# Kernel tuning notes

Hardware: AMD Instinct MI355X
Metric: run time of the kernel (lower is better)

The kernel has to match this reference:

```python
import jax, jax.numpy as jnp
import numpy as np

B, S, E = 2, 2048, 1024
H, D = 16, 64


def setup_inputs() -> dict:
    key = jax.random.key(0)
    ks = jax.random.split(key, 9)
    s_in = 1.0 / np.sqrt(E)
    s_out = 1.0 / np.sqrt(H * D)
    return {
        "x": jax.random.normal(ks[0], (B, S, E), dtype=jnp.float32),
        "W_q": jax.random.uniform(ks[1], (H, E, D), jnp.float32, -s_in, s_in),
        "b_q": jax.random.uniform(ks[2], (H, D), jnp.float32, -s_in, s_in),
        "W_k": jax.random.uniform(ks[3], (H, E, D), jnp.float32, -s_in, s_in),
        "b_k": jax.random.uniform(ks[4], (H, D), jnp.float32, -s_in, s_in),
        "W_v": jax.random.uniform(ks[5], (H, E, D), jnp.float32, -s_in, s_in),
        "b_v": jax.random.uniform(ks[6], (H, D), jnp.float32, -s_in, s_in),
        "W_o": jax.random.uniform(ks[7], (H * D, E), jnp.float32, -s_out, s_out),
        "b_o": jax.random.uniform(ks[8], (E,), jnp.float32, -s_out, s_out),
    }


def reference(x, W_q, b_q, W_k, b_k, W_v, b_v, W_o, b_o):
    # batched per-head projections: [B,S,E] x [H,E,D] -> [B,H,S,D]
    q = jnp.einsum("bse,hed->bhsd", x, W_q) + b_q[None, :, None, :]
    k = jnp.einsum("bse,hed->bhsd", x, W_k) + b_k[None, :, None, :]
    v = jnp.einsum("bse,hed->bhsd", x, W_v) + b_v[None, :, None, :]
    scale = 1.0 / jnp.sqrt(jnp.asarray(D, dtype=x.dtype))
    score = jnp.einsum("bhsd,bhtd->bhst", q, k) * scale  # [B,H,S,S]
    causal = jnp.tril(jnp.ones((S, S), dtype=bool))
    score = jnp.where(causal[None, None], score, -jnp.inf)
    w = jax.nn.softmax(score, axis=-1)
    o = jnp.einsum("bhst,bhtd->bhsd", w, v)  # [B,H,S,D]
    # concat heads along last dim (head-major order matches torch.cat)
    o = o.transpose(0, 2, 1, 3).reshape(B, S, H * D)
    # dropout is identity in eval mode
    return o @ W_o + b_o
```

## Files before the change

kernel.cpp:

```cpp
#include <hip/hip_runtime.h>


typedef __attribute__((ext_vector_type(8)))  __bf16 bf16x8;
typedef __attribute__((ext_vector_type(4)))  __bf16 bf16x4;
typedef __attribute__((ext_vector_type(2)))  __bf16 bf16x2;
typedef __attribute__((ext_vector_type(4)))  float  f32x4;
typedef __attribute__((ext_vector_type(16))) float  f32x16;
typedef __attribute__((ext_vector_type(2)))  unsigned int u32x2;
typedef __attribute__((ext_vector_type(4)))  unsigned int u32x4;

#define LOG2E 1.4426950408889634f
#define SM_SC (0.125f * LOG2E)
#define MBIAS (32.0f * SM_SC)

static __device__ __forceinline__ void gl2lds16(const void* g, void* l) {
    __builtin_amdgcn_global_load_lds(
        (__attribute__((address_space(1))) void*)(void*)g,
        (__attribute__((address_space(3))) void*)l, 16, 0, 0);
}

static __device__ __forceinline__ unsigned pku(float a, float b) {
    bf16x2 t = { (__bf16)a, (__bf16)b };
    return __builtin_bit_cast(unsigned, t);
}

__global__ void __launch_bounds__(256)
prep_all_kern(const float* __restrict__ x, const float* __restrict__ Wq,
              const float* __restrict__ Wk, const float* __restrict__ Wv,
              const float* __restrict__ bq, const float* __restrict__ bk,
              const float* __restrict__ bv, const float* __restrict__ Wo,
              __bf16* __restrict__ xb, __bf16* __restrict__ wt,
              float* __restrict__ bias, __bf16* __restrict__ wto) {
    __shared__ float T[64][65];
    const int t = threadIdx.x;
    const int bx = blockIdx.x;
    if (bx < 4096) {
        int i = (bx * 256 + t) * 4;
        f32x4 v = *(const f32x4*)(x + i);
        bf16x4 o = { (__bf16)v[0], (__bf16)v[1], (__bf16)v[2], (__bf16)v[3] };
        *(bf16x4*)(xb + i) = o;
    } else if (bx < 4864) {
        const int blk = bx - 4096;
        const int kt = blk & 15, ph = blk >> 4;
        const int h = ph & 15, p = ph >> 4;
        const float* W  = (p == 0) ? Wq : (p == 1) ? Wk : Wv;
        const float* bb = (p == 0) ? bq : (p == 1) ? bk : bv;
        #pragma unroll
        for (int i = 0; i < 4; ++i) {
            int flat = i * 1024 + t * 4;
            int kr = flat >> 6, d4 = flat & 63;
            f32x4 v = *(const f32x4*)(W + (h << 16) + ((kt * 64 + kr) << 6) + d4);
            T[kr][d4] = v[0]; T[kr][d4 + 1] = v[1]; T[kr][d4 + 2] = v[2]; T[kr][d4 + 3] = v[3];
        }
        __syncthreads();
        const int d = t >> 2, kq = (t & 3) << 4;
        bf16x8 o0, o1;
        #pragma unroll
        for (int j = 0; j < 8; ++j) o0[j] = (__bf16)T[kq + j][d];
        #pragma unroll
        for (int j = 0; j < 8; ++j) o1[j] = (__bf16)T[kq + 8 + j][d];
        __bf16* dst = wt + (((size_t)(p * 1024 + h * 64 + d)) << 10) + kt * 64 + kq;
        *(bf16x8*)dst = o0;
        *(bf16x8*)(dst + 8) = o1;
        if (kt == 0 && t < 64) bias[p * 1024 + h * 64 + t] = bb[h * 64 + t];
    } else {
        const int blk = bx - 4864;
        const int nt = blk & 15, ktile = blk >> 4;
        #pragma unroll
        for (int i = 0; i < 4; ++i) {
            int flat = i * 1024 + t * 4;
            int kr = flat >> 6, n4 = flat & 63;
            f32x4 v = *(const f32x4*)(Wo + ((size_t)(ktile * 64 + kr) << 10) + nt * 64 + n4);
            T[kr][n4] = v[0]; T[kr][n4 + 1] = v[1]; T[kr][n4 + 2] = v[2]; T[kr][n4 + 3] = v[3];
        }
        __syncthreads();
        const int n = t >> 2, kq = (t & 3) << 4;
        bf16x8 o0, o1;
        #pragma unroll
        for (int j = 0; j < 8; ++j) o0[j] = (__bf16)T[kq + j][n];
        #pragma unroll
        for (int j = 0; j < 8; ++j) o1[j] = (__bf16)T[kq + 8 + j][n];
        __bf16* dst = wto + (((size_t)(nt * 64 + n)) << 10) + ktile * 64 + kq;
        *(bf16x8*)dst = o0;
        *(bf16x8*)(dst + 8) = o1;
    }
}

template <int EPI>
__global__ void __launch_bounds__(256, 3)
gemm_bt(const __bf16* __restrict__ A, const __bf16* __restrict__ Bt,
        const float* __restrict__ bias,
        __bf16* __restrict__ outq, __bf16* __restrict__ outk, __bf16* __restrict__ outv,
        float* __restrict__ outf)
{
    __shared__ __align__(16) __bf16 As[128 * 64];
    __shared__ __align__(16) __bf16 Bs[128 * 64];
    const int tid = threadIdx.x;
    const int wid = tid >> 6, lane = tid & 63;
    const int r = lane & 15, g = lane >> 4;
    const int m0 = blockIdx.y << 7, n0 = blockIdx.x << 7;
    const int wr = wid >> 1, wc = wid & 1;
    f32x4 acc[4][4] = {};
    for (int k0 = 0; k0 < 1024; k0 += 64) {
        #pragma unroll
        for (int c = 0; c < 4; ++c) {
            int cq = (c * 4 + wid) * 64 + lane;
            int row = cq >> 3, ci = cq & 7;
            gl2lds16(A  + (((size_t)(m0 + row)) << 10) + k0 + ci * 8, As + (c * 4 + wid) * 512);
            gl2lds16(Bt + (((size_t)(n0 + row)) << 10) + k0 + ci * 8, Bs + (c * 4 + wid) * 512);
        }
        __syncthreads();
        bf16x8 af[2][4], bfr[2][4];
        #pragma unroll
        for (int kh = 0; kh < 2; ++kh)
            #pragma unroll
            for (int i = 0; i < 4; ++i) {
                af[kh][i]  = *(const bf16x8*)&As[(wr * 64 + i * 16 + r) * 64 + kh * 32 + g * 8];
                bfr[kh][i] = *(const bf16x8*)&Bs[(wc * 64 + i * 16 + r) * 64 + kh * 32 + g * 8];
            }
        #pragma unroll
        for (int kh = 0; kh < 2; ++kh)
            #pragma unroll
            for (int mi = 0; mi < 4; ++mi)
                #pragma unroll
                for (int ni = 0; ni < 4; ++ni)
                    acc[mi][ni] = __builtin_amdgcn_mfma_f32_16x16x32_bf16(
                        af[kh][mi], bfr[kh][ni], acc[mi][ni], 0, 0, 0);
        __syncthreads();
    }
    if (EPI == 0) {
        #pragma unroll
        for (int ni = 0; ni < 4; ++ni) {
            int n = n0 + wc * 64 + ni * 16 + r;
            float bv = bias[n];
            int p = n >> 10, rem = n & 1023, h = rem >> 6, d = rem & 63;
            #pragma unroll
            for (int mi = 0; mi < 4; ++mi) {
                int mb = m0 + wr * 64 + mi * 16 + g * 4;
                int b = mb >> 11, s = mb & 2047;
                f32x4 v = acc[mi][ni];
                if (p < 2) {
                    __bf16* dst = (p == 0) ? outq : outk;
                    size_t base = (((size_t)(b * 16 + h)) * 2048 + s) * 64 + d;
                    #pragma unroll
                    for (int j = 0; j < 4; ++j)
                        dst[base + (size_t)j * 64] = (__bf16)(v[j] + bv);
                } else {
                    bf16x4 pk = { (__bf16)(v[0] + bv), (__bf16)(v[1] + bv),
                                  (__bf16)(v[2] + bv), (__bf16)(v[3] + bv) };
                    *(bf16x4*)&outv[(((size_t)(b * 16 + h)) * 64 + d) * 2048 + s] = pk;
                }
            }
        }
    } else {
        #pragma unroll
        for (int ni = 0; ni < 4; ++ni) {
            int n = n0 + wc * 64 + ni * 16 + r;
            float bv = bias[n];
            #pragma unroll
            for (int mi = 0; mi < 4; ++mi) {
                int mb = m0 + wr * 64 + mi * 16 + g * 4;
                f32x4 v = acc[mi][ni];
                #pragma unroll
                for (int j = 0; j < 4; ++j)
                    outf[((size_t)(mb + j) << 10) + n] = v[j] + bv;
            }
        }
    }
}

__global__ void __launch_bounds__(256, 3)
attn_kern(const __bf16* __restrict__ q, const __bf16* __restrict__ k,
          const __bf16* __restrict__ vT, __bf16* __restrict__ pO0,
          __bf16* __restrict__ pO1, __bf16* __restrict__ pO2,
          __bf16* __restrict__ pO3, float* __restrict__ ml)
{
    __shared__ __align__(16) __bf16 Ks [2][64][72];
    __shared__ __align__(16) __bf16 VsT[2][64][72];
    const int tid = threadIdx.x, lane = tid & 63, w = tid >> 6;
    const int r31 = lane & 31, hi = lane >> 5;
    const int bid = blockIdx.x;
    const int rnk = bid >> 5, bh = bid & 31;
    const int j = 15 - (rnk >> 2), kvq = rnk & 3;
    const int b = bh >> 4, h = bh & 15;
    const __bf16* qh  = q  + ((size_t)bh << 17);
    const __bf16* khp = k  + ((size_t)bh << 17);
    const __bf16* vhp = vT + ((size_t)bh << 17);
    __bf16* pO = (kvq == 0) ? pO0 : (kvq == 1) ? pO1 : (kvq == 2) ? pO2 : pO3;
    const int srow = tid >> 3, sci = tid & 7;

    const int qb0 = j << 7;
    const int wrow0 = qb0 + w * 32;
    const int mg = wrow0 + r31;
    const int c2 = 2 * (j + 1);
    const int base = c2 >> 2, rem = c2 & 3;
    const int len = base + (kvq < rem ? 1 : 0);
    const int tbeg = kvq * base + min(kvq, rem);
    const int tend = tbeg + len;

    f32x16 oacc[2] = {};
    f32x16 lacc = {};

    if (len > 0) {
        bf16x8 qf[4];
        #pragma unroll
        for (int kk = 0; kk < 4; ++kk)
            qf[kk] = *(const bf16x8*)&qh[(size_t)mg * 64 + kk * 16 + hi * 8];
        bf16x8 onesf;
        #pragma unroll
        for (int jj = 0; jj < 8; ++jj) onesf[jj] = (__bf16)1.0f;

        #pragma unroll
        for (int it = 0; it < 2; ++it) {
            int row = srow + it * 32;
            *(bf16x8*)&Ks [0][row][sci * 8] = *(const bf16x8*)&khp[(size_t)(tbeg * 64 + row) * 64 + sci * 8];
            *(bf16x8*)&VsT[0][row][sci * 8] = *(const bf16x8*)&vhp[(size_t)row * 2048 + tbeg * 64 + sci * 8];
        }
        __syncthreads();

        for (int t = tbeg; t < tend; ++t) {
            const int cur = (t - tbeg) & 1, nxt = cur ^ 1;
            const int n0 = t << 6;
            const bool pre = (t + 1 < tend);
            bf16x8 nk[2], nv[2];
            if (pre) {
                int n1 = n0 + 64;
                #pragma unroll
                for (int it = 0; it < 2; ++it) {
                    int row = srow + it * 32;
                    nk[it] = *(const bf16x8*)&khp[(size_t)(n1 + row) * 64 + sci * 8];
                    nv[it] = *(const bf16x8*)&vhp[(size_t)row * 2048 + n1 + sci * 8];
                }
            }
            if (n0 <= wrow0 + 31) {
                f32x16 sacc[2] = {};
                #pragma unroll
                for (int kk = 0; kk < 4; ++kk) {
                    bf16x8 kf0 = *(const bf16x8*)&Ks[cur][r31]     [kk * 16 + hi * 8];
                    bf16x8 kf1 = *(const bf16x8*)&Ks[cur][32 + r31][kk * 16 + hi * 8];
                    sacc[0] = __builtin_amdgcn_mfma_f32_32x32x16_bf16(kf0, qf[kk], sacc[0], 0, 0, 0);
                    sacc[1] = __builtin_amdgcn_mfma_f32_32x32x16_bf16(kf1, qf[kk], sacc[1], 0, 0, 0);
                }
                if (n0 + 63 > wrow0) {
                    #pragma unroll
                    for (int nf = 0; nf < 2; ++nf)
                        #pragma unroll
                        for (int i = 0; i < 16; ++i) {
                            int n = n0 + nf * 32 + (i & 3) + 8 * (i >> 2) + 4 * hi;
                            if (n > mg) sacc[nf][i] = -3.0e38f;
                        }
                }
                #pragma unroll
                for (int nf = 0; nf < 2; ++nf)
                    #pragma unroll
                    for (int i = 0; i < 16; ++i)
                        sacc[nf][i] = exp2f(fmaf(sacc[nf][i], SM_SC, -MBIAS));
                #pragma unroll
                for (int nf = 0; nf < 2; ++nf) {
                    unsigned pk[8];
                    #pragma unroll
                    for (int jj = 0; jj < 8; ++jj)
                        pk[jj] = pku(sacc[nf][2 * jj], sacc[nf][2 * jj + 1]);
#if __has_builtin(__builtin_amdgcn_permlane32_swap)
                    u32x2 s02 = __builtin_amdgcn_permlane32_swap(pk[0], pk[2], false, false);
                    u32x2 s13 = __builtin_amdgcn_permlane32_swap(pk[1], pk[3], false, false);
                    u32x2 s46 = __builtin_amdgcn_permlane32_swap(pk[4], pk[6], false, false);
                    u32x2 s57 = __builtin_amdgcn_permlane32_swap(pk[5], pk[7], false, false);
                    u32x4 fw0 = { s02[0], s13[0], s02[1], s13[1] };
                    u32x4 fw1 = { s46[0], s57[0], s46[1], s57[1] };
#else
                    unsigned rxa = __shfl_xor(hi ? pk[0] : pk[2], 32);
                    unsigned rxb = __shfl_xor(hi ? pk[1] : pk[3], 32);
                    unsigned rxc = __shfl_xor(hi ? pk[4] : pk[6], 32);
                    unsigned rxd = __shfl_xor(hi ? pk[5] : pk[7], 32);
                    u32x4 fw0 = { hi ? rxa : pk[0], hi ? rxb : pk[1],
                                  hi ? pk[2] : rxa, hi ? pk[3] : rxb };
                    u32x4 fw1 = { hi ? rxc : pk[4], hi ? rxd : pk[5],
                                  hi ? pk[6] : rxc, hi ? pk[7] : rxd };
#endif
                    bf16x8 pf0 = __builtin_bit_cast(bf16x8, fw0);
                    bf16x8 pf1 = __builtin_bit_cast(bf16x8, fw1);
                    #pragma unroll
                    for (int kl = 0; kl < 2; ++kl) {
                        const bf16x8 pf = kl ? pf1 : pf0;
                        const int kk = nf * 2 + kl;
                        bf16x8 af0 = *(const bf16x8*)&VsT[cur][r31]     [kk * 16 + hi * 8];
                        bf16x8 af1 = *(const bf16x8*)&VsT[cur][32 + r31][kk * 16 + hi * 8];
                        oacc[0] = __builtin_amdgcn_mfma_f32_32x32x16_bf16(af0, pf, oacc[0], 0, 0, 0);
                        oacc[1] = __builtin_amdgcn_mfma_f32_32x32x16_bf16(af1, pf, oacc[1], 0, 0, 0);
                        lacc    = __builtin_amdgcn_mfma_f32_32x32x16_bf16(onesf, pf, lacc, 0, 0, 0);
                    }
                }
            }
            if (pre) {
                #pragma unroll
                for (int it = 0; it < 2; ++it) {
                    int row = srow + it * 32;
                    *(bf16x8*)&Ks [nxt][row][sci * 8] = nk[it];
                    *(bf16x8*)&VsT[nxt][row][sci * 8] = nv[it];
                }
            }
            __syncthreads();
        }
    }
    float lrun = lacc[0];
    float inv = (lrun > 0.f) ? 1.0f / lrun : 0.f;
    #pragma unroll
    for (int df = 0; df < 2; ++df)
        #pragma unroll
        for (int td = 0; td < 8; ++td) {
            bf16x2 pr = { (__bf16)(oacc[df][2 * td] * inv),
                          (__bf16)(oacc[df][2 * td + 1] * inv) };
            int d = df * 32 + 8 * (td >> 1) + 4 * hi + 2 * (td & 1);
            *(bf16x2*)&pO[((size_t)(b * 2048 + mg) << 10) + h * 64 + d] = pr;
        }
    if (hi == 0)
        ml[((size_t)(kvq * 32 + bh) << 11) + mg] = lrun;
}

__global__ void merge_kern(const __bf16* __restrict__ pO0, const __bf16* __restrict__ pO2,
                           const __bf16* __restrict__ pO3, const float* __restrict__ ml,
                           __bf16* __restrict__ ob)
{
    int i = blockIdx.x * 256 + threadIdx.x;
    int m = i >> 7, rem = i & 127, h = rem >> 3, d8 = (rem & 7) * 8;
    int bh = (m >> 11) * 16 + h, sr = m & 2047;
    size_t i0 = ((size_t)bh << 11) + sr;
    float c0 = ml[i0];
    float c1 = ml[65536 + i0];
    float c2 = ml[131072 + i0];
    float c3 = ml[196608 + i0];
    float inv = 1.0f / (c0 + c1 + c2 + c3);
    size_t off = (size_t)m * 1024 + h * 64 + d8;
    bf16x8 a0 = *(const bf16x8*)(pO0 + off);
    bf16x8 a1 = *(const bf16x8*)(ob + off);
    bf16x8 a2 = *(const bf16x8*)(pO2 + off);
    bf16x8 a3 = *(const bf16x8*)(pO3 + off);
    bf16x8 r;
    #pragma unroll
    for (int j = 0; j < 8; ++j)
        r[j] = (__bf16)((c0 * (float)a0[j] + c1 * (float)a1[j] +
                         c2 * (float)a2[j] + c3 * (float)a3[j]) * inv);
    *(bf16x8*)(ob + off) = r;
}

extern "C" void kernel_launch(void* const* d_in, const int* in_sizes, int n_in,
                              void* d_out, int out_size, void* d_ws, size_t ws_size,
                              hipStream_t stream) {
    const float* x  = (const float*)d_in[0];
    const float* Wq = (const float*)d_in[1];
    const float* bq = (const float*)d_in[2];
    const float* Wk = (const float*)d_in[3];
    const float* bk = (const float*)d_in[4];
    const float* Wv = (const float*)d_in[5];
    const float* bv = (const float*)d_in[6];
    const float* Wo = (const float*)d_in[7];
    const float* bo = (const float*)d_in[8];
    float* out = (float*)d_out;
    char* ws = (char*)d_ws;
    __bf16* xb    = (__bf16*)(ws + 0);
    __bf16* wtqkv = (__bf16*)(ws + 8388608);
    __bf16* wot   = (__bf16*)(ws + 14680064);
    float*  biasq = (float*) (ws + 16777216);
    __bf16* qb    = (__bf16*)(ws + 16793600);
    __bf16* kb    = (__bf16*)(ws + 25182208);
    __bf16* vtb   = (__bf16*)(ws + 33570816);
    __bf16* ob    = (__bf16*)(ws + 41959424);
    __bf16* pO0   = xb;
    __bf16* pO2   = (__bf16*)d_out;
    __bf16* pO3   = (__bf16*)d_out + 4194304;
    float*  mlbuf = (float*)(ws + 8388608);

    prep_all_kern<<<5120, 256, 0, stream>>>(x, Wq, Wk, Wv, bq, bk, bv, Wo,
                                            xb, wtqkv, biasq, wot);
    gemm_bt<0><<<dim3(24, 32), 256, 0, stream>>>(xb, wtqkv, biasq, qb, kb, vtb, nullptr);
    attn_kern<<<2048, 256, 0, stream>>>(qb, kb, vtb, pO0, ob, pO2, pO3, mlbuf);
    merge_kern<<<2048, 256, 0, stream>>>(pO0, pO2, pO3, mlbuf, ob);
    gemm_bt<1><<<dim3(8, 32), 256, 0, stream>>>(ob, wot, bo, nullptr, nullptr, nullptr, out);
}
```

Before: 118.4 us.

## Stage K/V tiles via direct global-to-LDS loads with XOR swizzle

Replaces the register-staged prefetch of K and V^T tiles with direct global_load_lds transfers into double-buffered LDS. An XOR column swizzle replaces the padded row layout so that MFMA operand reads stay free of bank conflicts. The smaller LDS footprint and lower register pressure let the launch bound rise to 4 blocks per CU. The risk is that the async LDS writes rely on the existing __syncthreads for ordering, so the waitcnt handling must be correct.

New measurement: 123.5 us. 1.04x slower.

```diff
diff --git a/kernel.cpp b/kernel.cpp
--- a/kernel.cpp
+++ b/kernel.cpp
@@ -169,14 +169,14 @@
     }
 }
 
-__global__ void __launch_bounds__(256, 3)
+__global__ void __launch_bounds__(256, 4)
 attn_kern(const __bf16* __restrict__ q, const __bf16* __restrict__ k,
           const __bf16* __restrict__ vT, __bf16* __restrict__ pO0,
           __bf16* __restrict__ pO1, __bf16* __restrict__ pO2,
           __bf16* __restrict__ pO3, float* __restrict__ ml)
 {
-    __shared__ __align__(16) __bf16 Ks [2][64][72];
-    __shared__ __align__(16) __bf16 VsT[2][64][72];
+    __shared__ __align__(16) __bf16 Ks [2][64][64];
+    __shared__ __align__(16) __bf16 VsT[2][64][64];
     const int tid = threadIdx.x, lane = tid & 63, w = tid >> 6;
     const int r31 = lane & 31, hi = lane >> 5;
     const int bid = blockIdx.x;
@@ -187,7 +187,6 @@
     const __bf16* khp = k  + ((size_t)bh << 17);
     const __bf16* vhp = vT + ((size_t)bh << 17);
     __bf16* pO = (kvq == 0) ? pO0 : (kvq == 1) ? pO1 : (kvq == 2) ? pO2 : pO3;
-    const int srow = tid >> 3, sci = tid & 7;
 
     const int qb0 = j << 7;
     const int wrow0 = qb0 + w * 32;
@@ -198,6 +197,8 @@
     const int tbeg = kvq * base + min(kvq, rem);
     const int tend = tbeg + len;
 
+    const int swz = r31 & 7;
+
     f32x16 oacc[2] = {};
     f32x16 lacc = {};
 
@@ -210,34 +211,35 @@
         #pragma unroll
         for (int jj = 0; jj < 8; ++jj) onesf[jj] = (__bf16)1.0f;
 
-        #pragma unroll
-        for (int it = 0; it < 2; ++it) {
-            int row = srow + it * 32;
-            *(bf16x8*)&Ks [0][row][sci * 8] = *(const bf16x8*)&khp[(size_t)(tbeg * 64 + row) * 64 + sci * 8];
-            *(bf16x8*)&VsT[0][row][sci * 8] = *(const bf16x8*)&vhp[(size_t)row * 2048 + tbeg * 64 + sci * 8];
-        }
+        auto stage = [&](int buf, int tile) {
+            const int n0s = tile << 6;
+            #pragma unroll
+            for (int it = 0; it < 2; ++it) {
+                const int cq0 = (w * 2 + it) * 64;
+                const int cq = cq0 + lane;
+                const int row = cq >> 3, c8 = cq & 7;
+                const int c8s = c8 ^ (row & 7);
+                gl2lds16(khp + (size_t)(n0s + row) * 64 + c8s * 8,
+                         (__bf16*)Ks  + buf * 4096 + cq0 * 8);
+                gl2lds16(vhp + (size_t)row * 2048 + n0s + c8s * 8,
+                         (__bf16*)VsT + buf * 4096 + cq0 * 8);
+            }
+        };
+
+        stage(0, tbeg);
         __syncthreads();
 
         for (int t = tbeg; t < tend; ++t) {
             const int cur = (t - tbeg) & 1, nxt = cur ^ 1;
             const int n0 = t << 6;
-            const bool pre = (t + 1 < tend);
-            bf16x8 nk[2], nv[2];
-            if (pre) {
-                int n1 = n0 + 64;
-                #pragma unroll
-                for (int it = 0; it < 2; ++it) {
-                    int row = srow + it * 32;
-                    nk[it] = *(const bf16x8*)&khp[(size_t)(n1 + row) * 64 + sci * 8];
-                    nv[it] = *(const bf16x8*)&vhp[(size_t)row * 2048 + n1 + sci * 8];
-                }
-            }
+            if (t + 1 < tend) stage(nxt, t + 1);
             if (n0 <= wrow0 + 31) {
                 f32x16 sacc[2] = {};
                 #pragma unroll
                 for (int kk = 0; kk < 4; ++kk) {
-                    bf16x8 kf0 = *(const bf16x8*)&Ks[cur][r31]     [kk * 16 + hi * 8];
-                    bf16x8 kf1 = *(const bf16x8*)&Ks[cur][32 + r31][kk * 16 + hi * 8];
+                    const int cs = ((kk * 2 + hi) ^ swz) * 8;
+                    bf16x8 kf0 = *(const bf16x8*)&Ks[cur][r31]     [cs];
+                    bf16x8 kf1 = *(const bf16x8*)&Ks[cur][32 + r31][cs];
                     sacc[0] = __builtin_amdgcn_mfma_f32_32x32x16_bf16(kf0, qf[kk], sacc[0], 0, 0, 0);
                     sacc[1] = __builtin_amdgcn_mfma_f32_32x32x16_bf16(kf1, qf[kk], sacc[1], 0, 0, 0);
                 }
@@ -284,20 +286,13 @@
                     for (int kl = 0; kl < 2; ++kl) {
                         const bf16x8 pf = kl ? pf1 : pf0;
                         const int kk = nf * 2 + kl;
-                        bf16x8 af0 = *(const bf16x8*)&VsT[cur][r31]     [kk * 16 + hi * 8];
-                        bf16x8 af1 = *(const bf16x8*)&VsT[cur][32 + r31][kk * 16 + hi * 8];
+                        const int cs = ((kk * 2 + hi) ^ swz) * 8;
+                        bf16x8 af0 = *(const bf16x8*)&VsT[cur][r31]     [cs];
+                        bf16x8 af1 = *(const bf16x8*)&VsT[cur][32 + r31][cs];
                         oacc[0] = __builtin_amdgcn_mfma_f32_32x32x16_bf16(af0, pf, oacc[0], 0, 0, 0);
                         oacc[1] = __builtin_amdgcn_mfma_f32_32x32x16_bf16(af1, pf, oacc[1], 0, 0, 0);
                         lacc    = __builtin_amdgcn_mfma_f32_32x32x16_bf16(onesf, pf, lacc, 0, 0, 0);
                     }
-                }
-            }
-            if (pre) {
-                #pragma unroll
-                for (int it = 0; it < 2; ++it) {
-                    int row = srow + it * 32;
-                    *(bf16x8*)&Ks [nxt][row][sci * 8] = nk[it];
-                    *(bf16x8*)&VsT[nxt][row][sci * 8] = nv[it];
                 }
             }
             __syncthreads();
```
